# Performance work log

Hardware: AMD Instinct MI355X
Metric: run time of the kernel (lower is better)

The kernel has to match this reference:

```python
import jax, jax.numpy as jnp
import numpy as np

B, N, E = 64, 256, 8192


def setup_inputs() -> dict:
    key = jax.random.key(0)
    k1, k2, k3, k4, k5 = jax.random.split(key, 5)
    P = jax.random.uniform(k1, (B, N, N), dtype=jnp.float32)
    d_error = jax.random.uniform(k2, (N, N), dtype=jnp.float32)
    edge_i = jax.random.randint(k3, (B, E), 0, N, dtype=jnp.int32)
    edge_j = jax.random.randint(k4, (B, E), 0, N, dtype=jnp.int32)
    edge_w = jax.random.uniform(k5, (B, E), dtype=jnp.float32)
    return {"P": P, "d_error": d_error, "edge_i": edge_i,
            "edge_j": edge_j, "edge_w": edge_w}


def reference(P, d_error, edge_i, edge_j, edge_w):
    # cost_e = P[b, i_e, :] @ d_error @ P[b, j_e, :]
    # Precompute Q = P @ d_error once, then gather per edge (memory-bound).
    Q = jnp.einsum('bin,nm->bim', P, d_error)            # [B, N, N]
    Qi = jnp.take_along_axis(Q, edge_i[:, :, None], axis=1)   # [B, E, N]
    Pj = jnp.take_along_axis(P, edge_j[:, :, None], axis=1)   # [B, E, N]
    cost = jnp.sum(Qi * Pj, axis=-1)                      # [B, E]
    sample_loss = jnp.sum(edge_w * cost, axis=-1)         # [B]
    sample_weight = jnp.maximum(jnp.sum(edge_w, axis=-1), 1e-8)
    # every sample has edges -> valid_samples == B, i.e. a mean over batch
    return jnp.mean(sample_loss / sample_weight)
```

## Files before the change

### kernel.cpp

```cpp
#include <hip/hip_runtime.h>
#include <hip/hip_bf16.h>

#define NN 256
#define EE 8192
#define SLD 40
#define TLD 264
#define SROWS 320

typedef __attribute__((ext_vector_type(8))) short bf16x8;
typedef __attribute__((ext_vector_type(4))) float f32x4;

__device__ __forceinline__ float bf2f(unsigned short h) {
  union { unsigned u; float f; } x; x.u = ((unsigned)h) << 16;
  return x.f;
}

__device__ __forceinline__ unsigned pack2(float x, float y) {
  union { __hip_bfloat162 h; unsigned u; } c;
  c.h = __float22bfloat162_rn(make_float2(x, y));
  return c.u;
}
__device__ __forceinline__ ushort4 cvt4f(float4 v) {
  union { ushort4 s; unsigned u[2]; } r;
  r.u[0] = pack2(v.x, v.y); r.u[1] = pack2(v.z, v.w);
  return r.s;
}
__device__ __forceinline__ ushort4 cvt4a(f32x4 v) {
  union { ushort4 s; unsigned u[2]; } r;
  r.u[0] = pack2(v[0], v[1]); r.u[1] = pack2(v[2], v[3]);
  return r.s;
}

__device__ __forceinline__ void barrier_lgkm() {
  asm volatile("s_waitcnt lgkmcnt(0)" ::: "memory");
  __builtin_amdgcn_s_barrier();
}

__global__ __launch_bounds__(512, 2) void fused(const float* __restrict__ P,
                                                const float* __restrict__ D,
                                                const int* __restrict__ ei,
                                                const int* __restrict__ ej,
                                                const float* __restrict__ ew,
                                                float* __restrict__ out) {
  __shared__ __align__(16) unsigned short Stage[2][SROWS * SLD];
  __shared__ __align__(16) unsigned short Tt[64 * TLD];
  __shared__ float red[16];

  const int tid = threadIdx.x;
  const int b = blockIdx.x >> 2;
  const int jt = blockIdx.x & 3;
  const int jBase = jt * 64;

  const int lane = tid & 63;
  const int wave = tid >> 6;
  const int wm = wave * 32;
  const int frm = lane & 15;
  const int fq = (lane >> 4) * 8;
  const int crow = (lane >> 4) * 4;
  const int ccol = lane & 15;

  const float4* Pb4 = (const float4*)(P + b * NN * NN);
  const float4* D4  = (const float4*)D;

  const int srow = tid >> 3;
  const int sc4  = tid & 7;

  float4 rd[2][4];
  float4 rp[2];

  auto loadStep = [&](int g, int set) {
    if (g < 8) {
#pragma unroll
      for (int i = 0; i < 4; ++i) rd[set][i] = D4[(srow + i * 64) * 64 + g * 8 + sc4];
      rp[set] = Pb4[(jBase + srow) * 64 + g * 8 + sc4];
    } else {
#pragma unroll
      for (int i = 0; i < 4; ++i) rd[set][i] = Pb4[(srow + i * 64) * 64 + (g - 8) * 8 + sc4];
    }
  };
  auto writeStep = [&](int buf, int g, int set) {
#pragma unroll
    for (int i = 0; i < 4; ++i)
      *(ushort4*)(&Stage[buf][(srow + i * 64) * SLD + sc4 * 4]) = cvt4f(rd[set][i]);
    if (g < 8)
      *(ushort4*)(&Stage[buf][(256 + srow) * SLD + sc4 * 4]) = cvt4f(rp[set]);
  };

  loadStep(0, 0);
  loadStep(1, 1);
  writeStep(0, 0, 0);
  barrier_lgkm();

  f32x4 acc1[2][4];
#pragma unroll
  for (int i = 0; i < 2; ++i)
#pragma unroll
    for (int j = 0; j < 4; ++j) acc1[i][j] = (f32x4){0.f, 0.f, 0.f, 0.f};

#pragma unroll
  for (int g = 0; g < 8; ++g) {
    const int cur = g & 1;
    bf16x8 af[2], bfr[4];
#pragma unroll
    for (int t = 0; t < 2; ++t)
      af[t] = *(const bf16x8*)(&Stage[cur][(wm + t * 16 + frm) * SLD + fq]);
#pragma unroll
    for (int t = 0; t < 4; ++t)
      bfr[t] = *(const bf16x8*)(&Stage[cur][(256 + t * 16 + frm) * SLD + fq]);
    writeStep(cur ^ 1, g + 1, (g + 1) & 1);
    loadStep(g + 2, g & 1);
#pragma unroll
    for (int tr = 0; tr < 2; ++tr)
#pragma unroll
      for (int tc = 0; tc < 4; ++tc)
        acc1[tr][tc] = __builtin_amdgcn_mfma_f32_16x16x32_bf16(af[tr], bfr[tc],
                                                               acc1[tr][tc], 0, 0, 0);
    if (g == 7) {
#pragma unroll
      for (int tr = 0; tr < 2; ++tr)
#pragma unroll
        for (int tc = 0; tc < 4; ++tc)
          *(ushort4*)(&Tt[(tc * 16 + ccol) * TLD + wm + tr * 16 + crow]) = cvt4a(acc1[tr][tc]);
    }
    barrier_lgkm();
  }

  const int4*   ei4 = (const int4*)(ei + b * EE);
  const int4*   ej4 = (const int4*)(ej + b * EE);
  const float4* ew4 = (const float4*)(ew + b * EE);
  int4 eii[4], ejj[4];
  float4 eww[4];
#pragma unroll
  for (int s = 0; s < 4; ++s) {
    eii[s] = ei4[s * 512 + tid];
    ejj[s] = ej4[s * 512 + tid];
    eww[s] = ew4[s * 512 + tid];
  }

  f32x4 acc2[2][4];
#pragma unroll
  for (int i = 0; i < 2; ++i)
#pragma unroll
    for (int j = 0; j < 4; ++j) acc2[i][j] = (f32x4){0.f, 0.f, 0.f, 0.f};

#pragma unroll
  for (int g2 = 0; g2 < 8; ++g2) {
    const int g = 8 + g2;
    const int cur = g & 1;
    bf16x8 af[2], bfr[4];
#pragma unroll
    for (int t = 0; t < 2; ++t)
      af[t] = *(const bf16x8*)(&Stage[cur][(wm + t * 16 + frm) * SLD + fq]);
#pragma unroll
    for (int t = 0; t < 4; ++t)
      bfr[t] = *(const bf16x8*)(&Tt[(t * 16 + frm) * TLD + g2 * 32 + fq]);
    if (g2 < 7) writeStep(cur ^ 1, g + 1, (g + 1) & 1);
    if (g2 < 6) loadStep(g + 2, g & 1);
#pragma unroll
    for (int tr = 0; tr < 2; ++tr)
#pragma unroll
      for (int tc = 0; tc < 4; ++tc)
        acc2[tr][tc] = __builtin_amdgcn_mfma_f32_16x16x32_bf16(af[tr], bfr[tc],
                                                               acc2[tr][tc], 0, 0, 0);
    barrier_lgkm();
  }

#pragma unroll
  for (int tr = 0; tr < 2; ++tr)
#pragma unroll
    for (int tc = 0; tc < 4; ++tc)
      *(ushort4*)(&Tt[(tc * 16 + ccol) * TLD + wm + tr * 16 + crow]) = cvt4a(acc2[tr][tc]);
  barrier_lgkm();

  float lsum = 0.f, wsum = 0.f;
#pragma unroll
  for (int s = 0; s < 4; ++s) {
    int4 ii = eii[s];
    int4 jj = ejj[s];
    float4 ww = eww[s];
    wsum += ww.x + ww.y + ww.z + ww.w;
    int jl;
    jl = jj.x - jBase; if ((unsigned)jl < 64u) lsum += ww.x * bf2f(Tt[jl * TLD + ii.x]);
    jl = jj.y - jBase; if ((unsigned)jl < 64u) lsum += ww.y * bf2f(Tt[jl * TLD + ii.y]);
    jl = jj.z - jBase; if ((unsigned)jl < 64u) lsum += ww.z * bf2f(Tt[jl * TLD + ii.z]);
    jl = jj.w - jBase; if ((unsigned)jl < 64u) lsum += ww.w * bf2f(Tt[jl * TLD + ii.w]);
  }
#pragma unroll
  for (int o = 32; o; o >>= 1) {
    lsum += __shfl_down(lsum, o);
    wsum += __shfl_down(wsum, o);
  }
  if (lane == 0) { red[wave] = lsum; red[8 + wave] = wsum; }
  barrier_lgkm();
  if (tid == 0) {
    float l = 0.f, w = 0.f;
#pragma unroll
    for (int i = 0; i < 8; ++i) { l += red[i]; w += red[8 + i]; }
    atomicAdd(out, l / (64.0f * fmaxf(w, 1e-8f)));
  }
}

extern "C" void kernel_launch(void* const* d_in, const int* in_sizes, int n_in,
                              void* d_out, int out_size, void* d_ws, size_t ws_size,
                              hipStream_t stream) {
  const float* P  = (const float*)d_in[0];
  const float* D  = (const float*)d_in[1];
  const int*   ei = (const int*)d_in[2];
  const int*   ej = (const int*)d_in[3];
  const float* ew = (const float*)d_in[4];
  float* out = (float*)d_out;

  fused<<<256, 512, 0, stream>>>(P, D, ei, ej, ew, out);
}
```

Before: 87.63 us.

## Pre-convert P and D to swizzled bf16 and stream tiles via global_load_lds

Adds a prep kernel that converts P and D to bf16 in a tiled, XOR-swizzled layout in workspace. The fused kernel then loads tiles straight into LDS with global_load_lds in a triple-buffered pipeline paced by vmcnt waits instead of per-tile barriers. The whole 64-row P slab is kept resident in LDS, block-to-batch mapping is permuted, and edge loads are deferred to overlap the second GEMM. This removes register staging and in-kernel conversion, at the cost of an extra launch, a full extra pass over P in memory, lower occupancy (one block per CU), and fragile hand-tuned waitcnt logic.

```diff
diff --git a/kernel.cpp b/kernel.cpp
--- a/kernel.cpp
+++ b/kernel.cpp
@@ -3,9 +3,7 @@
 
 #define NN 256
 #define EE 8192
-#define SLD 40
 #define TLD 264
-#define SROWS 320
 
 typedef __attribute__((ext_vector_type(8))) short bf16x8;
 typedef __attribute__((ext_vector_type(4))) float f32x4;
@@ -14,82 +12,105 @@
   union { unsigned u; float f; } x; x.u = ((unsigned)h) << 16;
   return x.f;
 }
-
 __device__ __forceinline__ unsigned pack2(float x, float y) {
   union { __hip_bfloat162 h; unsigned u; } c;
   c.h = __float22bfloat162_rn(make_float2(x, y));
   return c.u;
 }
-__device__ __forceinline__ ushort4 cvt4f(float4 v) {
-  union { ushort4 s; unsigned u[2]; } r;
-  r.u[0] = pack2(v.x, v.y); r.u[1] = pack2(v.z, v.w);
-  return r.s;
-}
 __device__ __forceinline__ ushort4 cvt4a(f32x4 v) {
   union { ushort4 s; unsigned u[2]; } r;
   r.u[0] = pack2(v[0], v[1]); r.u[1] = pack2(v[2], v[3]);
   return r.s;
 }
 
+template <int N> __device__ __forceinline__ void vwait() {
+  asm volatile("s_waitcnt vmcnt(%0)" :: "n"(N) : "memory");
+}
+__device__ __forceinline__ void lgkm0() {
+  asm volatile("s_waitcnt lgkmcnt(0)" ::: "memory");
+}
 __device__ __forceinline__ void barrier_lgkm() {
-  asm volatile("s_waitcnt lgkmcnt(0)" ::: "memory");
+  lgkm0();
   __builtin_amdgcn_s_barrier();
 }
-
-__global__ __launch_bounds__(512, 2) void fused(const float* __restrict__ P,
-                                                const float* __restrict__ D,
+__device__ __forceinline__ void glds16(const void* g, void* l) {
+  __builtin_amdgcn_global_load_lds(
+      (const __attribute__((address_space(1))) unsigned int*)g,
+      (__attribute__((address_space(3))) unsigned int*)l, 16, 0, 0);
+}
+
+__global__ __launch_bounds__(256) void prep(const float* __restrict__ P,
+                                            const float* __restrict__ D,
+                                            unsigned short* __restrict__ Dt,
+                                            unsigned short* __restrict__ Pt) {
+  const int gid = blockIdx.x * 256 + threadIdx.x;
+  const float4* Df4 = (const float4*)D;
+  const float4* Pf4 = (const float4*)P;
+  if (gid < 8192) {
+    const int d = gid;
+    const int cbp = d & 3, row = (d >> 2) & 255, g = d >> 10;
+    const int cb = cbp ^ (row & 3);
+    const int fi = row * 64 + g * 8 + cb * 2;
+    float4 a = Df4[fi], c = Df4[fi + 1];
+    uint4 o;
+    o.x = pack2(a.x, a.y); o.y = pack2(a.z, a.w);
+    o.z = pack2(c.x, c.y); o.w = pack2(c.z, c.w);
+    ((uint4*)Dt)[d] = o;
+  } else {
+    const int q = gid - 8192;
+    const int cbp = q & 3, row = (q >> 2) & 255, g = (q >> 10) & 7, bb = q >> 13;
+    const int cb = cbp ^ (row & 3);
+    const int fi = bb * 16384 + row * 64 + g * 8 + cb * 2;
+    float4 a = Pf4[fi], c = Pf4[fi + 1];
+    uint4 o;
+    o.x = pack2(a.x, a.y); o.y = pack2(a.z, a.w);
+    o.z = pack2(c.x, c.y); o.w = pack2(c.z, c.w);
+    ((uint4*)Pt)[q] = o;
+  }
+}
+
+__global__ __launch_bounds__(512, 1) void fused(const unsigned short* __restrict__ Pt,
+                                                const unsigned short* __restrict__ Dt,
                                                 const int* __restrict__ ei,
                                                 const int* __restrict__ ej,
                                                 const float* __restrict__ ew,
                                                 float* __restrict__ out) {
-  __shared__ __align__(16) unsigned short Stage[2][SROWS * SLD];
+  __shared__ __align__(16) unsigned short Bp[16384];
+  __shared__ __align__(16) unsigned short Stage[24576];
   __shared__ __align__(16) unsigned short Tt[64 * TLD];
   __shared__ float red[16];
 
+  const int p = blockIdx.x;
+  const int b  = (p & 7) * 8 + (p >> 5);
+  const int jt = (p >> 3) & 3;
+  const int jBase = jt * 64;
+
   const int tid = threadIdx.x;
-  const int b = blockIdx.x >> 2;
-  const int jt = blockIdx.x & 3;
-  const int jBase = jt * 64;
-
-  const int lane = tid & 63;
-  const int wave = tid >> 6;
-  const int wm = wave * 32;
-  const int frm = lane & 15;
-  const int fq = (lane >> 4) * 8;
-  const int crow = (lane >> 4) * 4;
-  const int ccol = lane & 15;
-
-  const float4* Pb4 = (const float4*)(P + b * NN * NN);
-  const float4* D4  = (const float4*)D;
-
-  const int srow = tid >> 3;
-  const int sc4  = tid & 7;
-
-  float4 rd[2][4];
-  float4 rp[2];
-
-  auto loadStep = [&](int g, int set) {
-    if (g < 8) {
-#pragma unroll
-      for (int i = 0; i < 4; ++i) rd[set][i] = D4[(srow + i * 64) * 64 + g * 8 + sc4];
-      rp[set] = Pb4[(jBase + srow) * 64 + g * 8 + sc4];
-    } else {
-#pragma unroll
-      for (int i = 0; i < 4; ++i) rd[set][i] = Pb4[(srow + i * 64) * 64 + (g - 8) * 8 + sc4];
-    }
+  const int lane = tid & 63, wave = tid >> 6, wm = wave * 32;
+  const int frm = lane & 15, fq = (lane >> 4) * 8;
+  const int crow = (lane >> 4) * 4, ccol = lane & 15;
+  const int XT = ((lane >> 4) ^ (lane & 3)) << 4;
+
+  const char* PtB = (const char*)Pt + b * 131072;
+  const char* DtB = (const char*)Dt;
+  char* StB = (char*)Stage;
+  char* BpB = (char*)Bp;
+
+  auto issueTile = [&](int tg) {
+    const char* src = (tg < 8 ? DtB + tg * 16384 : PtB + (tg - 8) * 16384) + wave * 2048;
+    char* dst = StB + (tg % 3) * 16384 + wave * 2048;
+#pragma unroll
+    for (int q = 0; q < 2; ++q)
+      glds16(src + q * 1024 + lane * 16, dst + q * 1024);
   };
-  auto writeStep = [&](int buf, int g, int set) {
-#pragma unroll
-    for (int i = 0; i < 4; ++i)
-      *(ushort4*)(&Stage[buf][(srow + i * 64) * SLD + sc4 * 4]) = cvt4f(rd[set][i]);
-    if (g < 8)
-      *(ushort4*)(&Stage[buf][(256 + srow) * SLD + sc4 * 4]) = cvt4f(rp[set]);
-  };
-
-  loadStep(0, 0);
-  loadStep(1, 1);
-  writeStep(0, 0, 0);
-  barrier_lgkm();
+
+#pragma unroll
+  for (int q = 0; q < 4; ++q)
+    glds16(PtB + wave * 16384 + jBase * 64 + q * 1024 + lane * 16,
+           BpB + wave * 4096 + q * 1024);
+  issueTile(0); issueTile(1); issueTile(2);
+  vwait<6>();
+  __builtin_amdgcn_s_barrier();
 
   f32x4 acc1[2][4];
 #pragma unroll
@@ -99,16 +120,17 @@
 
 #pragma unroll
   for (int g = 0; g < 8; ++g) {
-    const int cur = g & 1;
+    vwait<4>();
     bf16x8 af[2], bfr[4];
+    const char* tb = StB + (g % 3) * 16384;
 #pragma unroll
     for (int t = 0; t < 2; ++t)
-      af[t] = *(const bf16x8*)(&Stage[cur][(wm + t * 16 + frm) * SLD + fq]);
+      af[t] = *(const bf16x8*)(tb + (wm + t * 16 + frm) * 64 + XT);
 #pragma unroll
     for (int t = 0; t < 4; ++t)
-      bfr[t] = *(const bf16x8*)(&Stage[cur][(256 + t * 16 + frm) * SLD + fq]);
-    writeStep(cur ^ 1, g + 1, (g + 1) & 1);
-    loadStep(g + 2, g & 1);
+      bfr[t] = *(const bf16x8*)(BpB + g * 4096 + (t * 16 + frm) * 64 + XT);
+    lgkm0();
+    issueTile(g + 3);
 #pragma unroll
     for (int tr = 0; tr < 2; ++tr)
 #pragma unroll
@@ -122,48 +144,56 @@
         for (int tc = 0; tc < 4; ++tc)
           *(ushort4*)(&Tt[(tc * 16 + ccol) * TLD + wm + tr * 16 + crow]) = cvt4a(acc1[tr][tc]);
     }
-    barrier_lgkm();
-  }
-
+  }
+  barrier_lgkm();
+
+  f32x4 acc2[2][4];
+#pragma unroll
+  for (int i = 0; i < 2; ++i)
+#pragma unroll
+    for (int j = 0; j < 4; ++j) acc2[i][j] = (f32x4){0.f, 0.f, 0.f, 0.f};
+
+  int4 eii[4], ejj[4];
+  float4 eww[4];
   const int4*   ei4 = (const int4*)(ei + b * EE);
   const int4*   ej4 = (const int4*)(ej + b * EE);
   const float4* ew4 = (const float4*)(ew + b * EE);
-  int4 eii[4], ejj[4];
-  float4 eww[4];
-#pragma unroll
-  for (int s = 0; s < 4; ++s) {
-    eii[s] = ei4[s * 512 + tid];
-    ejj[s] = ej4[s * 512 + tid];
-    eww[s] = ew4[s * 512 + tid];
-  }
-
-  f32x4 acc2[2][4];
-#pragma unroll
-  for (int i = 0; i < 2; ++i)
-#pragma unroll
-    for (int j = 0; j < 4; ++j) acc2[i][j] = (f32x4){0.f, 0.f, 0.f, 0.f};
 
 #pragma unroll
   for (int g2 = 0; g2 < 8; ++g2) {
     const int g = 8 + g2;
-    const int cur = g & 1;
+    if (g == 13)      vwait<16>();
+    else if (g == 14) vwait<14>();
+    else if (g == 15) vwait<12>();
+    else              vwait<4>();
     bf16x8 af[2], bfr[4];
+    const char* tb = StB + (g % 3) * 16384;
 #pragma unroll
     for (int t = 0; t < 2; ++t)
-      af[t] = *(const bf16x8*)(&Stage[cur][(wm + t * 16 + frm) * SLD + fq]);
+      af[t] = *(const bf16x8*)(tb + (wm + t * 16 + frm) * 64 + XT);
 #pragma unroll
     for (int t = 0; t < 4; ++t)
       bfr[t] = *(const bf16x8*)(&Tt[(t * 16 + frm) * TLD + g2 * 32 + fq]);
-    if (g2 < 7) writeStep(cur ^ 1, g + 1, (g + 1) & 1);
-    if (g2 < 6) loadStep(g + 2, g & 1);
+    lgkm0();
+    if (g <= 12) issueTile(g + 3);
+    if (g == 12) {
+      asm volatile("" ::: "memory");
+#pragma unroll
+      for (int s = 0; s < 4; ++s) {
+        eii[s] = ei4[s * 512 + tid];
+        ejj[s] = ej4[s * 512 + tid];
+        eww[s] = ew4[s * 512 + tid];
+      }
+      asm volatile("" ::: "memory");
+    }
 #pragma unroll
     for (int tr = 0; tr < 2; ++tr)
 #pragma unroll
       for (int tc = 0; tc < 4; ++tc)
         acc2[tr][tc] = __builtin_amdgcn_mfma_f32_16x16x32_bf16(af[tr], bfr[tc],
                                                                acc2[tr][tc], 0, 0, 0);
-    barrier_lgkm();
-  }
+  }
+  barrier_lgkm();
 
 #pragma unroll
   for (int tr = 0; tr < 2; ++tr)
@@ -210,5 +240,9 @@
   const float* ew = (const float*)d_in[4];
   float* out = (float*)d_out;
 
-  fused<<<256, 512, 0, stream>>>(P, D, ei, ej, ew, out);
-}
+  unsigned short* Dt = (unsigned short*)d_ws;
+  unsigned short* Pt = (unsigned short*)((char*)d_ws + 131072);
+
+  prep<<<2080, 256, 0, stream>>>(P, D, Dt, Pt);
+  fused<<<256, 512, 0, stream>>>(Pt, Dt, ei, ej, ew, out);
+}
```

After: 85.50 us. 2.4% less time.
